# Kernel tuning notes

Measured on AMD Instinct MI355X. Metric: run time of the kernel, lower is better.

The kernel has to match this reference:

```python
import jax, jax.numpy as jnp
import numpy as np

N_ATOMS = 131072
NUM_GS = 128
HIDDEN = 512
N_MOL = 1024


def setup_inputs() -> dict:
    key = jax.random.key(0)
    ks = jax.random.split(key, 16)
    Gs = jax.random.normal(ks[0], (N_ATOMS, NUM_GS), dtype=jnp.float32)
    types = jax.random.randint(ks[1], (N_ATOMS,), 0, 2, dtype=jnp.int32)
    mol_id = jnp.sort(jax.random.randint(ks[2], (N_ATOMS,), 0, N_MOL, dtype=jnp.int32))

    def dense(k, fi, fo):
        return (jax.random.normal(k, (fi, fo), dtype=jnp.float32) / np.float32(np.sqrt(fi)))

    params = {}
    for i, t in enumerate(("A", "B")):
        base = 3 + i * 3
        params[f"W1_{t}"] = dense(ks[base], NUM_GS, HIDDEN)
        params[f"b1_{t}"] = jnp.zeros((HIDDEN,), jnp.float32)
        params[f"W2_{t}"] = dense(ks[base + 1], HIDDEN, HIDDEN)
        params[f"b2_{t}"] = jnp.zeros((HIDDEN,), jnp.float32)
        params[f"W3_{t}"] = dense(ks[base + 2], HIDDEN, 1)
        params[f"b3_{t}"] = jnp.zeros((1,), jnp.float32)
        params[f"off_{t}"] = jnp.zeros((1,), jnp.float32)
    return {"Gs": Gs, "types": types, "mol_id": mol_id, **params}


def _ann(G, W1, b1, W2, b2, W3, b3, off):
    # Atomic NN: two tanh hidden layers, linear scalar output + trainable offset
    h = jnp.tanh(G @ W1 + b1)
    h = jnp.tanh(h @ W2 + b2)
    return (h @ W3 + b3 + off)[:, 0]  # [N]


def reference(Gs, types, mol_id,
              W1_A, b1_A, W2_A, b2_A, W3_A, b3_A, off_A,
              W1_B, b1_B, W2_B, b2_B, W3_B, b3_B, off_B):
    # Per-type expert MLPs; dense-select is the math-equivalent of
    # dynamic_partition -> per-type ANN -> dynamic_stitch for 2 experts.
    eA = _ann(Gs, W1_A, b1_A, W2_A, b2_A, W3_A, b3_A, off_A)
    eB = _ann(Gs, W1_B, b1_B, W2_B, b2_B, W3_B, b3_B, off_B)
    atom_e = jnp.where(types == 0, eA, eB)  # [N_ATOMS]
    # Ragged per-molecule reduce_sum == segment_sum over sorted mol ids
    mol_e = jax.ops.segment_sum(atom_e, mol_id, num_segments=N_MOL)
    counts = jax.ops.segment_sum(jnp.ones_like(atom_e), mol_id, num_segments=N_MOL)
    energy_per_atom = mol_e / jnp.maximum(counts, 1.0)
    return energy_per_atom[:, None]  # [N_MOL, 1]
```

## Files before the change

### kernel.cpp

```cpp
#include <hip/hip_runtime.h>

typedef _Float16 half8  __attribute__((ext_vector_type(8)));
typedef _Float16 half4v __attribute__((ext_vector_type(4)));
typedef __fp16   fp16x2 __attribute__((ext_vector_type(2)));
typedef float    floatx16 __attribute__((ext_vector_type(16)));

#define N_ATOMS 131072
#define NUM_GS  128
#define HIDDEN  512
#define N_MOL   1024

#define BM      64
#define NB_SIDE (N_ATOMS / BM)
#define NT32    (HIDDEN / 32)
#define SH1_LD  (HIDDEN + 8)
#define SGH_LD  (NUM_GS + 8)

#define WS_CNT_OFF     0
#define WS_MOLSUM_OFF  1024
#define WS_PERM_OFF    9216
#define WS_W1FA_OFF    533504
#define WS_W1FB_OFF    664576
#define WS_W2FA_OFF    795648
#define WS_W2FB_OFF    1319936
#define WS_ZERO_BYTES  5120

__device__ __forceinline__ float fast_tanh(float x) {
    float e = exp2f(x * 2.8853900817779268f);
    float r = __builtin_amdgcn_rcpf(e + 1.0f);
    return fmaf(-2.0f, r, 1.0f);
}

__global__ __launch_bounds__(256)
void prep_kernel(const int* __restrict__ types,
                 const float* __restrict__ W1A, const float* __restrict__ W1B,
                 const float* __restrict__ W2A, const float* __restrict__ W2B,
                 int* __restrict__ cnt, int* __restrict__ perm,
                 _Float16* __restrict__ W1FA, _Float16* __restrict__ W1FB,
                 _Float16* __restrict__ W2FA, _Float16* __restrict__ W2FB) {
    __shared__ float tile[32][65];
    const int p   = blockIdx.x;
    const int tid = threadIdx.x;

    if (p < 512) {
        __shared__ int sCA[4];
        __shared__ int sBaseA, sBaseB;
        const int i    = p * 256 + tid;
        const int lane = tid & 63;
        const int w    = tid >> 6;
        const bool isA = (types[i] == 0);
        unsigned long long mask = __ballot(isA);
        unsigned long long lt   = ((unsigned long long)1 << lane) - 1;
        int rA = __popcll(mask & lt);
        if (lane == 0) sCA[w] = __popcll(mask);
        __syncthreads();
        if (tid == 0) {
            int tot = sCA[0] + sCA[1] + sCA[2] + sCA[3];
            sBaseA = atomicAdd(&cnt[0], tot);
            sBaseB = atomicAdd(&cnt[1], 256 - tot);
        }
        __syncthreads();
        int preA = 0;
        #pragma unroll
        for (int k = 0; k < 4; ++k) preA += (k < w) ? sCA[k] : 0;
        int preB = w * 64 - preA;
        int rB   = lane - rA;
        if (isA) perm[sBaseA + preA + rA] = i;
        else     perm[N_ATOMS - 1 - (sBaseB + preB + rB)] = i;
        return;
    }

    const float* src; _Float16* dst; int pb;
    if (p < 544)      { src = W1A; dst = W1FA; pb = p - 512; }
    else if (p < 576) { src = W1B; dst = W1FB; pb = p - 544; }
    else if (p < 704) { src = W2A; dst = W2FA; pb = p - 576; }
    else              { src = W2B; dst = W2FB; pb = p - 704; }
    const int bx = pb & 7;
    const int by = pb >> 3;
    const int n0 = bx * 64, k0 = by * 32;
    #pragma unroll
    for (int i = 0; i < 8; ++i) {
        int idx = tid + i * 256;
        int r = idx >> 6, c = idx & 63;
        tile[r][c] = src[(size_t)(k0 + r) * HIDDEN + n0 + c];
    }
    __syncthreads();
    const int w = tid >> 6, lane = tid & 63;
    const int l5 = lane & 31, h = lane >> 5;
    const int ks_l = w >> 1, nt_l = w & 1;
    half8 v;
    #pragma unroll
    for (int j = 0; j < 8; ++j)
        v[j] = (_Float16)tile[ks_l * 16 + h * 8 + j][nt_l * 32 + l5];
    const int ksg = by * 2 + ks_l;
    const int ntg = bx * 2 + nt_l;
    *(half8*)(dst + (((size_t)ksg * NT32 + ntg) * 64 + lane) * 8) = v;
}

__global__ __launch_bounds__(512, 4)
void mlp_kernel(const float* __restrict__ Gs,
                const int*   __restrict__ mol_id,
                const _Float16* __restrict__ W1FA, const _Float16* __restrict__ W2FA,
                const float* __restrict__ b1A, const float* __restrict__ b2A,
                const float* __restrict__ W3A, const float* __restrict__ b3A,
                const float* __restrict__ offA,
                const _Float16* __restrict__ W1FB, const _Float16* __restrict__ W2FB,
                const float* __restrict__ b1B, const float* __restrict__ b2B,
                const float* __restrict__ W3B, const float* __restrict__ b3B,
                const float* __restrict__ offB,
                const int* __restrict__ cnt, const int* __restrict__ perm,
                float* __restrict__ mol_sum) {
    __shared__ __align__(16) _Float16 sBuf[BM * SH1_LD];
    __shared__ int   sOrig[BM];
    __shared__ float sPart[8][BM];

    _Float16 (*sH1)[SH1_LD] = (_Float16(*)[SH1_LD])sBuf;
    _Float16 (*sGh)[SGH_LD] = (_Float16(*)[SGH_LD])sBuf;

    const int b     = blockIdx.x;
    const int nA    = cnt[0];
    const int sideB = (b >= NB_SIDE) ? 1 : 0;
    const int r0    = (sideB ? b - NB_SIDE : b) * BM;
    const int nSide = sideB ? (N_ATOMS - nA) : nA;
    if (r0 >= nSide) return;

    const _Float16 *W1F, *W2F;
    const float *b1, *b2, *W3;
    float b3off;
    if (!sideB) { W1F = W1FA; W2F = W2FA; b1 = b1A; b2 = b2A; W3 = W3A; b3off = b3A[0] + offA[0]; }
    else        { W1F = W1FB; W2F = W2FB; b1 = b1B; b2 = b2B; W3 = W3B; b3off = b3B[0] + offB[0]; }

    const int tid = threadIdx.x;
    if (tid < BM) {
        int r = r0 + tid;
        int orig = -1;
        if (r < nSide) orig = sideB ? perm[N_ATOMS - 1 - r] : perm[r];
        sOrig[tid] = orig;
    }
    __syncthreads();

    #pragma unroll
    for (int i = 0; i < 4; ++i) {
        int idx = tid + 512 * i;
        int row = idx >> 5;
        int c4  = idx & 31;
        int orig = sOrig[row];
        float4 v = make_float4(0.f, 0.f, 0.f, 0.f);
        if (orig >= 0) v = ((const float4*)(Gs + (size_t)orig * NUM_GS))[c4];
        union { half4v h4; fp16x2 h2[2]; } hu;
        hu.h2[0] = __builtin_amdgcn_cvt_pkrtz(v.x, v.y);
        hu.h2[1] = __builtin_amdgcn_cvt_pkrtz(v.z, v.w);
        *(half4v*)&sGh[row][c4 * 4] = hu.h4;
    }
    __syncthreads();

    const int lane = tid & 63;
    const int wid  = tid >> 6;
    const int l5   = lane & 31;
    const int h    = lane >> 5;

    floatx16 acc[2][2];

    #pragma unroll
    for (int nt = 0; nt < 2; ++nt)
        #pragma unroll
        for (int g = 0; g < 4; ++g) {
            const float4 bv = *(const float4*)&b1[wid * 64 + nt * 32 + g * 8 + h * 4];
            acc[0][nt][g * 4 + 0] = bv.x; acc[1][nt][g * 4 + 0] = bv.x;
            acc[0][nt][g * 4 + 1] = bv.y; acc[1][nt][g * 4 + 1] = bv.y;
            acc[0][nt][g * 4 + 2] = bv.z; acc[1][nt][g * 4 + 2] = bv.z;
            acc[0][nt][g * 4 + 3] = bv.w; acc[1][nt][g * 4 + 3] = bv.w;
        }

    #pragma unroll 2
    for (int ks = 0; ks < NUM_GS / 16; ++ks) {
        half8 gb[2];
        #pragma unroll
        for (int mt = 0; mt < 2; ++mt)
            gb[mt] = *(const half8*)&sGh[mt * 32 + l5][ks * 16 + h * 8];
        #pragma unroll
        for (int nt = 0; nt < 2; ++nt) {
            const int ntile = wid * 2 + nt;
            half8 wa = *(const half8*)(W1F + (((size_t)ks * NT32 + ntile) * 64 + lane) * 8);
            #pragma unroll
            for (int mt = 0; mt < 2; ++mt)
                acc[mt][nt] = __builtin_amdgcn_mfma_f32_32x32x16_f16(wa, gb[mt], acc[mt][nt], 0, 0, 0);
        }
    }
    __syncthreads();

    #pragma unroll
    for (int mt = 0; mt < 2; ++mt)
        #pragma unroll
        for (int nt = 0; nt < 2; ++nt)
            #pragma unroll
            for (int g = 0; g < 4; ++g) {
                float t0 = fast_tanh(acc[mt][nt][g * 4 + 0]);
                float t1 = fast_tanh(acc[mt][nt][g * 4 + 1]);
                float t2 = fast_tanh(acc[mt][nt][g * 4 + 2]);
                float t3 = fast_tanh(acc[mt][nt][g * 4 + 3]);
                union { half4v h4; fp16x2 h2[2]; } hu;
                hu.h2[0] = __builtin_amdgcn_cvt_pkrtz(t0, t1);
                hu.h2[1] = __builtin_amdgcn_cvt_pkrtz(t2, t3);
                *(half4v*)&sH1[mt * 32 + l5][wid * 64 + nt * 32 + g * 8 + h * 4] = hu.h4;
            }
    __syncthreads();

    #pragma unroll
    for (int nt = 0; nt < 2; ++nt)
        #pragma unroll
        for (int g = 0; g < 4; ++g) {
            const float4 bv = *(const float4*)&b2[wid * 64 + nt * 32 + g * 8 + h * 4];
            acc[0][nt][g * 4 + 0] = bv.x; acc[1][nt][g * 4 + 0] = bv.x;
            acc[0][nt][g * 4 + 1] = bv.y; acc[1][nt][g * 4 + 1] = bv.y;
            acc[0][nt][g * 4 + 2] = bv.z; acc[1][nt][g * 4 + 2] = bv.z;
            acc[0][nt][g * 4 + 3] = bv.w; acc[1][nt][g * 4 + 3] = bv.w;
        }

    #pragma unroll 2
    for (int ks = 0; ks < HIDDEN / 16; ++ks) {
        half8 hb[2];
        #pragma unroll
        for (int mt = 0; mt < 2; ++mt)
            hb[mt] = *(const half8*)&sH1[mt * 32 + l5][ks * 16 + h * 8];
        #pragma unroll
        for (int nt = 0; nt < 2; ++nt) {
            const int ntile = wid * 2 + nt;
            half8 wa = *(const half8*)(W2F + (((size_t)ks * NT32 + ntile) * 64 + lane) * 8);
            #pragma unroll
            for (int mt = 0; mt < 2; ++mt)
                acc[mt][nt] = __builtin_amdgcn_mfma_f32_32x32x16_f16(wa, hb[mt], acc[mt][nt], 0, 0, 0);
        }
    }

    float4 w3v[2][4];
    #pragma unroll
    for (int nt = 0; nt < 2; ++nt)
        #pragma unroll
        for (int g = 0; g < 4; ++g)
            w3v[nt][g] = *(const float4*)&W3[wid * 64 + nt * 32 + g * 8 + h * 4];

    float p[2] = {0.f, 0.f};
    #pragma unroll
    for (int mt = 0; mt < 2; ++mt)
        #pragma unroll
        for (int nt = 0; nt < 2; ++nt)
            #pragma unroll
            for (int g = 0; g < 4; ++g) {
                p[mt] = fmaf(fast_tanh(acc[mt][nt][g * 4 + 0]), w3v[nt][g].x, p[mt]);
                p[mt] = fmaf(fast_tanh(acc[mt][nt][g * 4 + 1]), w3v[nt][g].y, p[mt]);
                p[mt] = fmaf(fast_tanh(acc[mt][nt][g * 4 + 2]), w3v[nt][g].z, p[mt]);
                p[mt] = fmaf(fast_tanh(acc[mt][nt][g * 4 + 3]), w3v[nt][g].w, p[mt]);
            }
    #pragma unroll
    for (int mt = 0; mt < 2; ++mt) {
        float v = p[mt];
        v += __shfl_xor(v, 32, 64);
        if (lane < 32) sPart[wid][mt * 32 + lane] = v;
    }
    __syncthreads();
    if (tid < BM) {
        int orig = sOrig[tid];
        if (orig >= 0) {
            float e = b3off;
            #pragma unroll
            for (int w = 0; w < 8; ++w) e += sPart[w][tid];
            atomicAdd(&mol_sum[mol_id[orig]], e);
        }
    }
}

__global__ void finalize_kernel(const float* __restrict__ mol_sum,
                                const int* __restrict__ mol_id,
                                float* __restrict__ out) {
    int m = blockIdx.x * blockDim.x + threadIdx.x;
    if (m >= N_MOL) return;
    int lo0 = 0, hi0 = N_ATOMS;
    while (lo0 < hi0) { int mid = (lo0 + hi0) >> 1; if (mol_id[mid] < m) lo0 = mid + 1; else hi0 = mid; }
    int lo1 = lo0, hi1 = N_ATOMS;
    while (lo1 < hi1) { int mid = (lo1 + hi1) >> 1; if (mol_id[mid] < m + 1) lo1 = mid + 1; else hi1 = mid; }
    float c = (float)(lo1 - lo0);
    out[m] = mol_sum[m] / fmaxf(c, 1.0f);
}

extern "C" void kernel_launch(void* const* d_in, const int* in_sizes, int n_in,
                              void* d_out, int out_size, void* d_ws, size_t ws_size,
                              hipStream_t stream) {
    const float* Gs     = (const float*)d_in[0];
    const int*   types  = (const int*)d_in[1];
    const int*   mol_id = (const int*)d_in[2];
    const float* W1A = (const float*)d_in[3];
    const float* b1A = (const float*)d_in[4];
    const float* W2A = (const float*)d_in[5];
    const float* b2A = (const float*)d_in[6];
    const float* W3A = (const float*)d_in[7];
    const float* b3A = (const float*)d_in[8];
    const float* oA  = (const float*)d_in[9];
    const float* W1B = (const float*)d_in[10];
    const float* b1B = (const float*)d_in[11];
    const float* W2B = (const float*)d_in[12];
    const float* b2B = (const float*)d_in[13];
    const float* W3B = (const float*)d_in[14];
    const float* b3B = (const float*)d_in[15];
    const float* oB  = (const float*)d_in[16];

    char* ws = (char*)d_ws;
    int*      cnt     = (int*)(ws + WS_CNT_OFF);
    float*    mol_sum = (float*)(ws + WS_MOLSUM_OFF);
    int*      perm    = (int*)(ws + WS_PERM_OFF);
    _Float16* W1FA    = (_Float16*)(ws + WS_W1FA_OFF);
    _Float16* W1FB    = (_Float16*)(ws + WS_W1FB_OFF);
    _Float16* W2FA    = (_Float16*)(ws + WS_W2FA_OFF);
    _Float16* W2FB    = (_Float16*)(ws + WS_W2FB_OFF);
    float* out = (float*)d_out;

    hipMemsetAsync(d_ws, 0, WS_ZERO_BYTES, stream);
    prep_kernel<<<832, 256, 0, stream>>>(types, W1A, W1B, W2A, W2B,
                                         cnt, perm,
                                         W1FA, W1FB, W2FA, W2FB);
    mlp_kernel<<<2 * NB_SIDE, 512, 0, stream>>>(
        Gs, mol_id,
        W1FA, W2FA, b1A, b2A, W3A, b3A, oA,
        W1FB, W2FB, b1B, b2B, W3B, b3B, oB,
        cnt, perm, mol_sum);
    finalize_kernel<<<(N_MOL + 255) / 256, 256, 0, stream>>>(mol_sum, mol_id, out);
}
```

Before: 280.6 us.

## Double atom tile to 128 rows and double-buffer weight fragment loads

Raises the per-block atom tile from 64 to 128 rows, so each weight fragment fetched from global memory feeds four MFMA row tiles instead of two, halving weight traffic per atom. The K loops are restructured to prefetch the next step's weight fragments into alternate registers while the current step computes. The larger accumulator set (8 floatx16) raises register pressure, so launch bounds are lowered to 2 blocks per CU, and shared memory per block roughly doubles, which reduces occupancy and latency hiding.

```diff
diff --git a/kernel.cpp b/kernel.cpp
--- a/kernel.cpp
+++ b/kernel.cpp
@@ -10,7 +10,7 @@
 #define HIDDEN  512
 #define N_MOL   1024
 
-#define BM      64
+#define BM      128
 #define NB_SIDE (N_ATOMS / BM)
 #define NT32    (HIDDEN / 32)
 #define SH1_LD  (HIDDEN + 8)
@@ -97,7 +97,7 @@
     *(half8*)(dst + (((size_t)ksg * NT32 + ntg) * 64 + lane) * 8) = v;
 }
 
-__global__ __launch_bounds__(512, 4)
+__global__ __launch_bounds__(512, 2)
 void mlp_kernel(const float* __restrict__ Gs,
                 const int*   __restrict__ mol_id,
                 const _Float16* __restrict__ W1FA, const _Float16* __restrict__ W2FA,
@@ -140,7 +140,7 @@
     __syncthreads();
 
     #pragma unroll
-    for (int i = 0; i < 4; ++i) {
+    for (int i = 0; i < 8; ++i) {
         int idx = tid + 512 * i;
         int row = idx >> 5;
         int c4  = idx & 31;
@@ -159,38 +159,56 @@
     const int l5   = lane & 31;
     const int h    = lane >> 5;
 
-    floatx16 acc[2][2];
+    floatx16 acc[4][2];
 
     #pragma unroll
     for (int nt = 0; nt < 2; ++nt)
         #pragma unroll
         for (int g = 0; g < 4; ++g) {
             const float4 bv = *(const float4*)&b1[wid * 64 + nt * 32 + g * 8 + h * 4];
-            acc[0][nt][g * 4 + 0] = bv.x; acc[1][nt][g * 4 + 0] = bv.x;
-            acc[0][nt][g * 4 + 1] = bv.y; acc[1][nt][g * 4 + 1] = bv.y;
-            acc[0][nt][g * 4 + 2] = bv.z; acc[1][nt][g * 4 + 2] = bv.z;
-            acc[0][nt][g * 4 + 3] = bv.w; acc[1][nt][g * 4 + 3] = bv.w;
-        }
-
-    #pragma unroll 2
-    for (int ks = 0; ks < NUM_GS / 16; ++ks) {
-        half8 gb[2];
-        #pragma unroll
-        for (int mt = 0; mt < 2; ++mt)
-            gb[mt] = *(const half8*)&sGh[mt * 32 + l5][ks * 16 + h * 8];
-        #pragma unroll
-        for (int nt = 0; nt < 2; ++nt) {
-            const int ntile = wid * 2 + nt;
-            half8 wa = *(const half8*)(W1F + (((size_t)ks * NT32 + ntile) * 64 + lane) * 8);
-            #pragma unroll
-            for (int mt = 0; mt < 2; ++mt)
-                acc[mt][nt] = __builtin_amdgcn_mfma_f32_32x32x16_f16(wa, gb[mt], acc[mt][nt], 0, 0, 0);
-        }
-    }
-    __syncthreads();
-
-    #pragma unroll
-    for (int mt = 0; mt < 2; ++mt)
+            #pragma unroll
+            for (int mt = 0; mt < 4; ++mt) {
+                acc[mt][nt][g * 4 + 0] = bv.x;
+                acc[mt][nt][g * 4 + 1] = bv.y;
+                acc[mt][nt][g * 4 + 2] = bv.z;
+                acc[mt][nt][g * 4 + 3] = bv.w;
+            }
+        }
+
+    #define LOADW(WF, dstv, ks)                                                   \
+        {                                                                         \
+            dstv[0] = *(const half8*)((WF) + (((size_t)(ks) * NT32 + wid * 2 + 0) * 64 + lane) * 8); \
+            dstv[1] = *(const half8*)((WF) + (((size_t)(ks) * NT32 + wid * 2 + 1) * 64 + lane) * 8); \
+        }
+    #define COMPUTE(SRC, wav, ks)                                                 \
+        {                                                                         \
+            half8 fb[4];                                                          \
+            _Pragma("unroll")                                                     \
+            for (int mt = 0; mt < 4; ++mt)                                        \
+                fb[mt] = *(const half8*)&SRC[mt * 32 + l5][(ks) * 16 + h * 8];    \
+            _Pragma("unroll")                                                     \
+            for (int nt = 0; nt < 2; ++nt)                                        \
+                _Pragma("unroll")                                                 \
+                for (int mt = 0; mt < 4; ++mt)                                    \
+                    acc[mt][nt] = __builtin_amdgcn_mfma_f32_32x32x16_f16(         \
+                        wav[nt], fb[mt], acc[mt][nt], 0, 0, 0);                   \
+        }
+
+    {
+        half8 waA[2], waB[2];
+        LOADW(W1F, waA, 0);
+        #pragma unroll
+        for (int ks = 0; ks < NUM_GS / 16; ks += 2) {
+            LOADW(W1F, waB, ks + 1);
+            COMPUTE(sGh, waA, ks);
+            if (ks + 2 < NUM_GS / 16) LOADW(W1F, waA, ks + 2);
+            COMPUTE(sGh, waB, ks + 1);
+        }
+    }
+    __syncthreads();
+
+    #pragma unroll
+    for (int mt = 0; mt < 4; ++mt)
         #pragma unroll
         for (int nt = 0; nt < 2; ++nt)
             #pragma unroll
@@ -211,27 +229,28 @@
         #pragma unroll
         for (int g = 0; g < 4; ++g) {
             const float4 bv = *(const float4*)&b2[wid * 64 + nt * 32 + g * 8 + h * 4];
-            acc[0][nt][g * 4 + 0] = bv.x; acc[1][nt][g * 4 + 0] = bv.x;
-            acc[0][nt][g * 4 + 1] = bv.y; acc[1][nt][g * 4 + 1] = bv.y;
-            acc[0][nt][g * 4 + 2] = bv.z; acc[1][nt][g * 4 + 2] = bv.z;
-            acc[0][nt][g * 4 + 3] = bv.w; acc[1][nt][g * 4 + 3] = bv.w;
-        }
-
-    #pragma unroll 2
-    for (int ks = 0; ks < HIDDEN / 16; ++ks) {
-        half8 hb[2];
-        #pragma unroll
-        for (int mt = 0; mt < 2; ++mt)
-            hb[mt] = *(const half8*)&sH1[mt * 32 + l5][ks * 16 + h * 8];
-        #pragma unroll
-        for (int nt = 0; nt < 2; ++nt) {
-            const int ntile = wid * 2 + nt;
-            half8 wa = *(const half8*)(W2F + (((size_t)ks * NT32 + ntile) * 64 + lane) * 8);
-            #pragma unroll
-            for (int mt = 0; mt < 2; ++mt)
-                acc[mt][nt] = __builtin_amdgcn_mfma_f32_32x32x16_f16(wa, hb[mt], acc[mt][nt], 0, 0, 0);
-        }
-    }
+            #pragma unroll
+            for (int mt = 0; mt < 4; ++mt) {
+                acc[mt][nt][g * 4 + 0] = bv.x;
+                acc[mt][nt][g * 4 + 1] = bv.y;
+                acc[mt][nt][g * 4 + 2] = bv.z;
+                acc[mt][nt][g * 4 + 3] = bv.w;
+            }
+        }
+
+    {
+        half8 waA[2], waB[2];
+        LOADW(W2F, waA, 0);
+        #pragma unroll 2
+        for (int ks = 0; ks < HIDDEN / 16; ks += 2) {
+            LOADW(W2F, waB, ks + 1);
+            COMPUTE(sH1, waA, ks);
+            if (ks + 2 < HIDDEN / 16) LOADW(W2F, waA, ks + 2);
+            COMPUTE(sH1, waB, ks + 1);
+        }
+    }
+    #undef LOADW
+    #undef COMPUTE
 
     float4 w3v[2][4];
     #pragma unroll
@@ -240,9 +259,9 @@
         for (int g = 0; g < 4; ++g)
             w3v[nt][g] = *(const float4*)&W3[wid * 64 + nt * 32 + g * 8 + h * 4];
 
-    float p[2] = {0.f, 0.f};
-    #pragma unroll
-    for (int mt = 0; mt < 2; ++mt)
+    float p[4] = {0.f, 0.f, 0.f, 0.f};
+    #pragma unroll
+    for (int mt = 0; mt < 4; ++mt)
         #pragma unroll
         for (int nt = 0; nt < 2; ++nt)
             #pragma unroll
@@ -253,7 +272,7 @@
                 p[mt] = fmaf(fast_tanh(acc[mt][nt][g * 4 + 3]), w3v[nt][g].w, p[mt]);
             }
     #pragma unroll
-    for (int mt = 0; mt < 2; ++mt) {
+    for (int mt = 0; mt < 4; ++mt) {
         float v = p[mt];
         v += __shfl_xor(v, 32, 64);
         if (lane < 32) sPart[wid][mt * 32 + lane] = v;
```

Measured after the change: 314.2 us. 1.12x slower.
